# Optimization experiments

Hardware: AMD Instinct MI355X
Metric: run time of the kernel (lower is better)

## Reference

```python
import jax, jax.numpy as jnp
import numpy as np

EPS = 1e-5
LEAK = 0.33  # scn LeakyReLU default leakiness


def leaky(x):
    return jnp.where(x > 0, x, LEAK * x)


def subm_conv(feat, idx, mask, w):
    # feat: [N,C], idx: [N,K] int, mask: [N,K] bool, w: [K,Cin,Cout]
    g = feat[idx] * mask[..., None]          # [N,K,C] gather of active neighbors
    return jnp.einsum('nkc,kcd->nd', g, w)   # [N,Cout]


def batch_norm(x, gamma, beta):
    # scn BatchNormalization in training mode: batch stats over active sites
    m = x.mean(axis=0)
    v = x.var(axis=0)
    return (x - m) * jax.lax.rsqrt(v + EPS) * gamma + beta


def setup_inputs() -> dict:
    key = jax.random.key(0)
    ks = jax.random.split(key, 8)
    N, K, C, B = 131072, 9, 64, 4
    features = jax.random.normal(ks[0], (N, C), dtype=jnp.float32)
    neighbor_idx = jax.random.randint(ks[1], (N, K), 0, N, dtype=jnp.int32)
    # center offset always points at self (submanifold conv semantics)
    neighbor_idx = neighbor_idx.at[:, K // 2].set(jnp.arange(N, dtype=jnp.int32))
    neighbor_mask = jax.random.randint(ks[2], (N, K), 0, 2) > 0
    neighbor_mask = neighbor_mask.at[:, K // 2].set(True)
    scale = 1.0 / np.sqrt(K * C)
    conv1_w = jax.random.normal(ks[3], (B, K, C, C), dtype=jnp.float32) * scale
    conv2_w = jax.random.normal(ks[4], (B, K, C, C), dtype=jnp.float32) * scale
    bn1_gamma = jnp.ones((B, C), dtype=jnp.float32)
    bn1_beta = jnp.zeros((B, C), dtype=jnp.float32)
    bn2_gamma = jnp.ones((B, C), dtype=jnp.float32)
    bn2_beta = jnp.zeros((B, C), dtype=jnp.float32)
    return {
        'features': features, 'neighbor_idx': neighbor_idx, 'neighbor_mask': neighbor_mask,
        'conv1_w': conv1_w, 'bn1_gamma': bn1_gamma, 'bn1_beta': bn1_beta,
        'conv2_w': conv2_w, 'bn2_gamma': bn2_gamma, 'bn2_beta': bn2_beta,
    }


def reference(features, neighbor_idx, neighbor_mask, conv1_w, bn1_gamma, bn1_beta,
              conv2_w, bn2_gamma, bn2_beta):
    x = features
    n_blocks = conv1_w.shape[0]
    for b in range(n_blocks):
        residual = x
        out = subm_conv(x, neighbor_idx, neighbor_mask, conv1_w[b])
        out = leaky(batch_norm(out, bn1_gamma[b], bn1_beta[b]))
        out = subm_conv(out, neighbor_idx, neighbor_mask, conv2_w[b])
        out = batch_norm(out, bn2_gamma[b], bn2_beta[b])
        x = leaky(out + residual)
    return x
```

## Files before the change

kernel.cpp:

```cpp
#include <hip/hip_runtime.h>
#include <hip/hip_bf16.h>
#include <stdint.h>

#define NROWS 131072
#define EPSBN 1e-5f
#define LEAKK 0.33f

typedef __bf16 bf16x8_t __attribute__((ext_vector_type(8)));
typedef float  f32x4_t  __attribute__((ext_vector_type(4)));

__device__ __forceinline__ float leaky_f(float x) { return fmaxf(x, LEAKK * x); }

#define GLDS16(g, l)                                                          \
    __builtin_amdgcn_global_load_lds(                                         \
        (const __attribute__((address_space(1))) void*)(g),                   \
        (__attribute__((address_space(3))) void*)(l), 16, 0, 0)

#define WAIT_VM18 0x4F72
#define WAIT_VM10 0x0F7A
#define WAIT_VM8  0x0F78
#define WAIT_VM0  0x0F70
#define CFENCE() asm volatile("" ::: "memory")

__global__ __launch_bounds__(256, 2) void conv_kernel(
    const __bf16* __restrict__ src,
    const int* __restrict__ cidxT,
    const __bf16* __restrict__ wt,
    __bf16* __restrict__ dst,
    float* __restrict__ stat_out)
{
    __shared__ char Ab[2][32768];
    __shared__ char Bb[2][8192];

    const int tid  = threadIdx.x;
    const int lane = tid & 63;
    const int wv   = tid >> 6;
    const int quad = lane >> 4;
    const int l15  = lane & 15;
    const int row0 = blockIdx.x << 8;
    const int srow = tid >> 3;
    const int cg   = (tid & 7) ^ (srow & 7);
    const int ldsl = (tid & 192) << 4;
    const int sxor = l15 & 7;

    const char* srcb = (const char*)src;
    const char* wtb  = (const char*)wt;

    f32x4_t acc[4][4];
#pragma unroll
    for (int mt = 0; mt < 4; ++mt)
#pragma unroll
        for (int nt = 0; nt < 4; ++nt)
            acc[mt][nt] = (f32x4_t){0.f, 0.f, 0.f, 0.f};

    int ix[2][8];
#pragma unroll
    for (int i = 0; i < 8; ++i) ix[0][i] = cidxT[row0 + (i << 5) + srow];
    CFENCE();
#pragma unroll
    for (int i = 0; i < 8; ++i) ix[1][i] = cidxT[NROWS + row0 + (i << 5) + srow];
    CFENCE();
    __builtin_amdgcn_s_waitcnt(WAIT_VM8);
#pragma unroll
    for (int i = 0; i < 8; ++i)
        GLDS16(srcb + ((size_t)ix[0][i] << 7) + (cg << 4), &Ab[0][(i << 12) + ldsl]);
#pragma unroll
    for (int i = 0; i < 2; ++i)
        GLDS16(wtb + (((i << 5) + srow) << 7) + (cg << 4), &Bb[0][(i << 12) + ldsl]);
    CFENCE();

#pragma unroll
    for (int k = 0; k < 9; ++k) {
        const int cur = k & 1, nxt = cur ^ 1;
        if (k < 7) {
#pragma unroll
            for (int i = 0; i < 8; ++i)
                ix[k & 1][i] = cidxT[(k + 2) * NROWS + row0 + (i << 5) + srow];
        }
        CFENCE();
        if (k < 7)       __builtin_amdgcn_s_waitcnt(WAIT_VM18);
        else if (k == 7) __builtin_amdgcn_s_waitcnt(WAIT_VM10);
        if (k < 8) {
            const int* ixu = ix[(k + 1) & 1];
#pragma unroll
            for (int i = 0; i < 8; ++i)
                GLDS16(srcb + ((size_t)ixu[i] << 7) + (cg << 4),
                       &Ab[nxt][(i << 12) + ldsl]);
#pragma unroll
            for (int i = 0; i < 2; ++i)
                GLDS16(wtb + ((size_t)(k + 1) << 13) + (((i << 5) + srow) << 7) + (cg << 4),
                       &Bb[nxt][(i << 12) + ldsl]);
        }
        CFENCE();
        if (k < 7)       __builtin_amdgcn_s_waitcnt(WAIT_VM18);
        else if (k == 7) __builtin_amdgcn_s_waitcnt(WAIT_VM10);
        else             __builtin_amdgcn_s_waitcnt(WAIT_VM0);
        __builtin_amdgcn_s_barrier();
        bf16x8_t af[4][2], bq[4][2];
#pragma unroll
        for (int ks = 0; ks < 2; ++ks) {
            const int slot = ((quad | (ks << 2)) ^ sxor) << 4;
#pragma unroll
            for (int mt = 0; mt < 4; ++mt) {
                int m = (wv << 6) + (mt << 4) + l15;
                af[mt][ks] = *(const bf16x8_t*)&Ab[cur][(m << 7) + slot];
            }
#pragma unroll
            for (int nt = 0; nt < 4; ++nt) {
                int d = (nt << 4) + l15;
                bq[nt][ks] = *(const bf16x8_t*)&Bb[cur][(d << 7) + slot];
            }
        }
#pragma unroll
        for (int ks = 0; ks < 2; ++ks)
#pragma unroll
            for (int mt = 0; mt < 4; ++mt)
#pragma unroll
                for (int nt = 0; nt < 4; ++nt)
                    acc[mt][nt] = __builtin_amdgcn_mfma_f32_16x16x32_bf16(
                        af[mt][ks], bq[nt][ks], acc[mt][nt], 0, 0, 0);
        __builtin_amdgcn_s_barrier();
    }

#pragma unroll
    for (int mt = 0; mt < 4; ++mt) {
        int rowb = row0 + (wv << 6) + (mt << 4) + (quad << 2);
#pragma unroll
        for (int nt = 0; nt < 4; ++nt) {
            int col = (nt << 4) + l15;
#pragma unroll
            for (int r = 0; r < 4; ++r)
                dst[((size_t)(rowb + r) << 6) + col] = (__bf16)acc[mt][nt][r];
        }
    }
    float* red = (float*)Bb[1];
    __syncthreads();
    if (tid < 128) red[tid] = 0.f;
    __syncthreads();
#pragma unroll
    for (int nt = 0; nt < 4; ++nt) {
        float s = 0.f, q = 0.f;
#pragma unroll
        for (int mt = 0; mt < 4; ++mt)
#pragma unroll
            for (int r = 0; r < 4; ++r) { float v = acc[mt][nt][r]; s += v; q += v * v; }
        s += __shfl_xor(s, 16); s += __shfl_xor(s, 32);
        q += __shfl_xor(q, 16); q += __shfl_xor(q, 32);
        if (lane < 16) {
            atomicAdd(&red[(nt << 4) + lane], s);
            atomicAdd(&red[64 + (nt << 4) + lane], q);
        }
    }
    __syncthreads();
    if (tid < 128) atomicAdd(&stat_out[tid], red[tid]);
}

__global__ __launch_bounds__(256) void bnact_kernel(
    __bf16* __restrict__ y, const float* __restrict__ stat,
    const float* __restrict__ gamma, const float* __restrict__ beta)
{
    __shared__ float sc[64], sh[64];
    int tid = threadIdx.x;
    if (tid < 64) {
        float m = stat[tid] * (1.f / NROWS);
        float v = stat[64 + tid] * (1.f / NROWS) - m * m;
        float s = gamma[tid] * rsqrtf(v + EPSBN);
        sc[tid] = s;
        sh[tid] = beta[tid] - m * s;
    }
    __syncthreads();
    size_t base = ((((size_t)blockIdx.x << 8) | tid) << 3);
    int c0 = (int)(base & 63);
    bf16x8_t hv = *(bf16x8_t*)(y + base);
#pragma unroll
    for (int j = 0; j < 8; ++j) {
        float f = (float)hv[j];
        f = leaky_f(f * sc[c0 + j] + sh[c0 + j]);
        hv[j] = (__bf16)f;
    }
    *(bf16x8_t*)(y + base) = hv;
}

__global__ __launch_bounds__(256) void resid_kernel(
    const __bf16* __restrict__ z, const float* __restrict__ xin,
    float* __restrict__ xf, __bf16* __restrict__ xh, float* __restrict__ dout,
    const float* __restrict__ stat, const float* __restrict__ gamma,
    const float* __restrict__ beta, int isfinal)
{
    __shared__ float sc[64], sh[64];
    int tid = threadIdx.x;
    if (tid < 64) {
        float m = stat[tid] * (1.f / NROWS);
        float v = stat[64 + tid] * (1.f / NROWS) - m * m;
        float s = gamma[tid] * rsqrtf(v + EPSBN);
        sc[tid] = s;
        sh[tid] = beta[tid] - m * s;
    }
    __syncthreads();
    size_t base = ((((size_t)blockIdx.x << 8) | tid) << 3);
    int c0 = (int)(base & 63);
    bf16x8_t zv = *(const bf16x8_t*)(z + base);
    float4 xa = *(const float4*)(xin + base);
    float4 xb = *(const float4*)(xin + base + 4);
    float o[8];
#pragma unroll
    for (int j = 0; j < 8; ++j) {
        float xv = (j < 4) ? (&xa.x)[j] : (&xb.x)[j - 4];
        o[j] = leaky_f((float)zv[j] * sc[c0 + j] + sh[c0 + j] + xv);
    }
    if (isfinal) {
        *(float4*)(dout + base)     = make_float4(o[0], o[1], o[2], o[3]);
        *(float4*)(dout + base + 4) = make_float4(o[4], o[5], o[6], o[7]);
    } else {
        *(float4*)(xf + base)     = make_float4(o[0], o[1], o[2], o[3]);
        *(float4*)(xf + base + 4) = make_float4(o[4], o[5], o[6], o[7]);
        bf16x8_t h;
#pragma unroll
        for (int j = 0; j < 8; ++j) h[j] = (__bf16)o[j];
        *(bf16x8_t*)(xh + base) = h;
    }
}

__global__ __launch_bounds__(256) void prep_kernel(
    const float* __restrict__ feat, const float* __restrict__ w1,
    const float* __restrict__ w2, const int* __restrict__ nidx,
    const unsigned char* __restrict__ mraw,
    __bf16* __restrict__ fh, __bf16* __restrict__ yh,
    __bf16* __restrict__ wtp, int* __restrict__ cidxT,
    float* __restrict__ stats)
{
    size_t t = ((size_t)blockIdx.x << 8) | threadIdx.x;
    if (t < 1024) stats[t] = 0.f;
    if (t < 64) {
        fh[(size_t)NROWS * 64 + t] = (__bf16)0.f;
        yh[(size_t)NROWS * 64 + t] = (__bf16)0.f;
    }
    if (t < 1048576) {
        size_t i = t << 3;
        float4 a = *(const float4*)(feat + i);
        float4 b = *(const float4*)(feat + i + 4);
        bf16x8_t h;
        h[0] = (__bf16)a.x; h[1] = (__bf16)a.y; h[2] = (__bf16)a.z; h[3] = (__bf16)a.w;
        h[4] = (__bf16)b.x; h[5] = (__bf16)b.y; h[6] = (__bf16)b.z; h[7] = (__bf16)b.w;
        *(bf16x8_t*)(fh + i) = h;
    }
    if (t < 294912) {
        int o = (int)t;
        int c = o & 63, d = (o >> 6) & 63;
        int kk = o >> 12;
        int k = kk % 9, bb = (kk / 9) & 3, cv = kk / 36;
        const float* w = cv ? w2 : w1;
        float v = w[((size_t)((bb * 9 + k) * 64 + c) << 6) + d];
        wtp[o] = (__bf16)v;
    }
    if (t < 1179648) {
        int k = (int)(t >> 17), n = (int)(t & 131071);
        bool bytes_enc = (mraw[13] != 0);
        int e = n * 9 + k;
        bool m = bytes_enc ? (mraw[e] != 0) : (((const unsigned int*)mraw)[e] != 0u);
        cidxT[t] = m ? nidx[e] : NROWS;
    }
}

extern "C" void kernel_launch(void* const* d_in, const int* in_sizes, int n_in,
                              void* d_out, int out_size, void* d_ws, size_t ws_size,
                              hipStream_t stream) {
    const float* feat = (const float*)d_in[0];
    const int* nidx = (const int*)d_in[1];
    const unsigned char* mraw = (const unsigned char*)d_in[2];
    const float* w1 = (const float*)d_in[3];
    const float* g1 = (const float*)d_in[4];
    const float* b1 = (const float*)d_in[5];
    const float* w2 = (const float*)d_in[6];
    const float* g2 = (const float*)d_in[7];
    const float* b2 = (const float*)d_in[8];
    float* out = (float*)d_out;

    char* ws = (char*)d_ws;
    float*  xf    = (float*)ws;
    __bf16* xh    = (__bf16*)(ws + 33554432);
    __bf16* yh    = (__bf16*)(ws + 50331904);
    __bf16* zh    = (__bf16*)(ws + 67109376);
    __bf16* wtp   = (__bf16*)(ws + 83886592);
    float*  stats = (float*)(ws + 84476416);
    int*    cidxT = (int*)(ws + 84480512);

    prep_kernel<<<4608, 256, 0, stream>>>(feat, w1, w2, nidx, mraw,
                                          xh, yh, wtp, cidxT, stats);

    for (int b = 0; b < 4; ++b) {
        conv_kernel<<<512, 256, 0, stream>>>(
            xh, cidxT, wtp + (size_t)b * 9 * 4096,
            yh, stats + (size_t)(2 * b) * 128);
        bnact_kernel<<<4096, 256, 0, stream>>>(
            yh, stats + (size_t)(2 * b) * 128, g1 + b * 64, b1 + b * 64);
        conv_kernel<<<512, 256, 0, stream>>>(
            yh, cidxT, wtp + (size_t)(4 + b) * 9 * 4096,
            zh, stats + (size_t)(2 * b + 1) * 128);
        resid_kernel<<<4096, 256, 0, stream>>>(
            zh, (b == 0) ? feat : xf, xf, xh, out,
            stats + (size_t)(2 * b + 1) * 128, g2 + b * 64, b2 + b * 64,
            (b == 3) ? 1 : 0);
    }
}
```

Measured before the change: 418.2 us.

## Shrink conv tile to 64 rows and deepen gather pipeline to five stages

```diff
diff --git a/kernel.cpp b/kernel.cpp
--- a/kernel.cpp
+++ b/kernel.cpp
@@ -16,10 +16,12 @@
         (const __attribute__((address_space(1))) void*)(g),                   \
         (__attribute__((address_space(3))) void*)(l), 16, 0, 0)
 
-#define WAIT_VM18 0x4F72
-#define WAIT_VM10 0x0F7A
-#define WAIT_VM8  0x0F78
-#define WAIT_VM0  0x0F70
+#define WAIT_VM16  0x4F70
+#define WAIT_VM12  0x0F7C
+#define WAIT_VM8   0x0F78
+#define WAIT_VM4   0x0F74
+#define WAIT_VM0   0x0F70
+#define WAIT_LGKM0 0xC07F
 #define CFENCE() asm volatile("" ::: "memory")
 
 __global__ __launch_bounds__(256, 2) void conv_kernel(
@@ -29,111 +31,103 @@
     __bf16* __restrict__ dst,
     float* __restrict__ stat_out)
 {
-    __shared__ char Ab[2][32768];
-    __shared__ char Bb[2][8192];
+    __shared__ char SL[5][16384];
 
     const int tid  = threadIdx.x;
     const int lane = tid & 63;
     const int wv   = tid >> 6;
     const int quad = lane >> 4;
     const int l15  = lane & 15;
-    const int row0 = blockIdx.x << 8;
+    const int row0 = blockIdx.x << 6;
     const int srow = tid >> 3;
     const int cg   = (tid & 7) ^ (srow & 7);
-    const int ldsl = (tid & 192) << 4;
+    const int ldsw = (tid & 192) << 4;
     const int sxor = l15 & 7;
 
     const char* srcb = (const char*)src;
     const char* wtb  = (const char*)wt;
 
-    f32x4_t acc[4][4];
-#pragma unroll
-    for (int mt = 0; mt < 4; ++mt)
-#pragma unroll
-        for (int nt = 0; nt < 4; ++nt)
-            acc[mt][nt] = (f32x4_t){0.f, 0.f, 0.f, 0.f};
-
-    int ix[2][8];
-#pragma unroll
-    for (int i = 0; i < 8; ++i) ix[0][i] = cidxT[row0 + (i << 5) + srow];
+    int ix[9][2];
+#pragma unroll
+    for (int k = 0; k < 9; ++k)
+#pragma unroll
+        for (int i = 0; i < 2; ++i)
+            ix[k][i] = cidxT[k * NROWS + row0 + (i << 5) + srow];
     CFENCE();
-#pragma unroll
-    for (int i = 0; i < 8; ++i) ix[1][i] = cidxT[NROWS + row0 + (i << 5) + srow];
-    CFENCE();
-    __builtin_amdgcn_s_waitcnt(WAIT_VM8);
-#pragma unroll
-    for (int i = 0; i < 8; ++i)
-        GLDS16(srcb + ((size_t)ix[0][i] << 7) + (cg << 4), &Ab[0][(i << 12) + ldsl]);
-#pragma unroll
-    for (int i = 0; i < 2; ++i)
-        GLDS16(wtb + (((i << 5) + srow) << 7) + (cg << 4), &Bb[0][(i << 12) + ldsl]);
-    CFENCE();
+
+    f32x4_t acc[4];
+#pragma unroll
+    for (int nt = 0; nt < 4; ++nt) acc[nt] = (f32x4_t){0.f, 0.f, 0.f, 0.f};
+
+#pragma unroll
+    for (int s = 0; s < 5; ++s) {
+#pragma unroll
+        for (int i = 0; i < 2; ++i)
+            GLDS16(srcb + ((size_t)ix[s][i] << 7) + (cg << 4),
+                   &SL[s][(i << 12) + ldsw]);
+#pragma unroll
+        for (int i = 0; i < 2; ++i)
+            GLDS16(wtb + ((size_t)s << 13) + (i << 12) + ((tid >> 3) << 7) + (cg << 4),
+                   &SL[s][8192 + (i << 12) + ldsw]);
+        CFENCE();
+    }
 
 #pragma unroll
     for (int k = 0; k < 9; ++k) {
-        const int cur = k & 1, nxt = cur ^ 1;
-        if (k < 7) {
-#pragma unroll
-            for (int i = 0; i < 8; ++i)
-                ix[k & 1][i] = cidxT[(k + 2) * NROWS + row0 + (i << 5) + srow];
-        }
-        CFENCE();
-        if (k < 7)       __builtin_amdgcn_s_waitcnt(WAIT_VM18);
-        else if (k == 7) __builtin_amdgcn_s_waitcnt(WAIT_VM10);
-        if (k < 8) {
-            const int* ixu = ix[(k + 1) & 1];
-#pragma unroll
-            for (int i = 0; i < 8; ++i)
-                GLDS16(srcb + ((size_t)ixu[i] << 7) + (cg << 4),
-                       &Ab[nxt][(i << 12) + ldsl]);
-#pragma unroll
-            for (int i = 0; i < 2; ++i)
-                GLDS16(wtb + ((size_t)(k + 1) << 13) + (((i << 5) + srow) << 7) + (cg << 4),
-                       &Bb[nxt][(i << 12) + ldsl]);
-        }
-        CFENCE();
-        if (k < 7)       __builtin_amdgcn_s_waitcnt(WAIT_VM18);
-        else if (k == 7) __builtin_amdgcn_s_waitcnt(WAIT_VM10);
+        if (k < 5)       __builtin_amdgcn_s_waitcnt(WAIT_VM16);
+        else if (k == 5) __builtin_amdgcn_s_waitcnt(WAIT_VM12);
+        else if (k == 6) __builtin_amdgcn_s_waitcnt(WAIT_VM8);
+        else if (k == 7) __builtin_amdgcn_s_waitcnt(WAIT_VM4);
         else             __builtin_amdgcn_s_waitcnt(WAIT_VM0);
         __builtin_amdgcn_s_barrier();
-        bf16x8_t af[4][2], bq[4][2];
+        CFENCE();
+
+        const char* As = SL[k % 5];
+        const char* Bs = As + 8192;
+        bf16x8_t af[2], bq[4][2];
 #pragma unroll
         for (int ks = 0; ks < 2; ++ks) {
             const int slot = ((quad | (ks << 2)) ^ sxor) << 4;
-#pragma unroll
-            for (int mt = 0; mt < 4; ++mt) {
-                int m = (wv << 6) + (mt << 4) + l15;
-                af[mt][ks] = *(const bf16x8_t*)&Ab[cur][(m << 7) + slot];
-            }
-#pragma unroll
-            for (int nt = 0; nt < 4; ++nt) {
-                int d = (nt << 4) + l15;
-                bq[nt][ks] = *(const bf16x8_t*)&Bb[cur][(d << 7) + slot];
-            }
+            af[ks] = *(const bf16x8_t*)(As + (((wv << 4) + l15) << 7) + slot);
+#pragma unroll
+            for (int nt = 0; nt < 4; ++nt)
+                bq[nt][ks] = *(const bf16x8_t*)(Bs + (((nt << 4) + l15) << 7) + slot);
         }
 #pragma unroll
         for (int ks = 0; ks < 2; ++ks)
 #pragma unroll
-            for (int mt = 0; mt < 4; ++mt)
-#pragma unroll
-                for (int nt = 0; nt < 4; ++nt)
-                    acc[mt][nt] = __builtin_amdgcn_mfma_f32_16x16x32_bf16(
-                        af[mt][ks], bq[nt][ks], acc[mt][nt], 0, 0, 0);
-        __builtin_amdgcn_s_barrier();
-    }
-
-#pragma unroll
-    for (int mt = 0; mt < 4; ++mt) {
-        int rowb = row0 + (wv << 6) + (mt << 4) + (quad << 2);
-#pragma unroll
-        for (int nt = 0; nt < 4; ++nt) {
-            int col = (nt << 4) + l15;
-#pragma unroll
-            for (int r = 0; r < 4; ++r)
-                dst[((size_t)(rowb + r) << 6) + col] = (__bf16)acc[mt][nt][r];
+            for (int nt = 0; nt < 4; ++nt)
+                acc[nt] = __builtin_amdgcn_mfma_f32_16x16x32_bf16(
+                    af[ks], bq[nt][ks], acc[nt], 0, 0, 0);
+
+        if (k < 4) {
+            CFENCE();
+            __builtin_amdgcn_s_waitcnt(WAIT_LGKM0);
+            __builtin_amdgcn_s_barrier();
+            CFENCE();
+            const int s = k + 5;
+#pragma unroll
+            for (int i = 0; i < 2; ++i)
+                GLDS16(srcb + ((size_t)ix[s][i] << 7) + (cg << 4),
+                       &SL[k % 5][(i << 12) + ldsw]);
+#pragma unroll
+            for (int i = 0; i < 2; ++i)
+                GLDS16(wtb + ((size_t)s << 13) + (i << 12) + ((tid >> 3) << 7) + (cg << 4),
+                       &SL[k % 5][8192 + (i << 12) + ldsw]);
+            CFENCE();
         }
     }
-    float* red = (float*)Bb[1];
+
+#pragma unroll
+    for (int nt = 0; nt < 4; ++nt) {
+        int rowb = row0 + (wv << 4) + (quad << 2);
+        int col  = (nt << 4) + l15;
+#pragma unroll
+        for (int r = 0; r < 4; ++r)
+            dst[((size_t)(rowb + r) << 6) + col] = (__bf16)acc[nt][r];
+    }
+
+    float* red = (float*)SL[0];
     __syncthreads();
     if (tid < 128) red[tid] = 0.f;
     __syncthreads();
@@ -141,9 +135,7 @@
     for (int nt = 0; nt < 4; ++nt) {
         float s = 0.f, q = 0.f;
 #pragma unroll
-        for (int mt = 0; mt < 4; ++mt)
-#pragma unroll
-            for (int r = 0; r < 4; ++r) { float v = acc[mt][nt][r]; s += v; q += v * v; }
+        for (int r = 0; r < 4; ++r) { float v = acc[nt][r]; s += v; q += v * v; }
         s += __shfl_xor(s, 16); s += __shfl_xor(s, 32);
         q += __shfl_xor(q, 16); q += __shfl_xor(q, 32);
         if (lane < 16) {
@@ -289,12 +281,12 @@
                                           xh, yh, wtp, cidxT, stats);
 
     for (int b = 0; b < 4; ++b) {
-        conv_kernel<<<512, 256, 0, stream>>>(
+        conv_kernel<<<2048, 256, 0, stream>>>(
             xh, cidxT, wtp + (size_t)b * 9 * 4096,
             yh, stats + (size_t)(2 * b) * 128);
         bnact_kernel<<<4096, 256, 0, stream>>>(
             yh, stats + (size_t)(2 * b) * 128, g1 + b * 64, b1 + b * 64);
-        conv_kernel<<<512, 256, 0, stream>>>(
+        conv_kernel<<<2048, 256, 0, stream>>>(
             yh, cidxT, wtp + (size_t)(4 + b) * 9 * 4096,
             zh, stats + (size_t)(2 * b + 1) * 128);
         resid_kernel<<<4096, 256, 0, stream>>>(
```

After: 663.2 us. 58.6% more time.
